# Optimization experiments

Hardware: AMD Instinct MI355X
Metric: run time of the kernel (lower is better)

Reference implementation:

```python
import jax, jax.numpy as jnp
import numpy as np


def setup_inputs() -> dict:
    key = jax.random.key(0)
    k0, k1, k2, k3, k4 = jax.random.split(key, 5)
    B, S, D, E, H = 2, 4096, 1024, 8, 512
    x = jax.random.normal(k0, (B, S, D), jnp.float32)
    w_router = jax.random.normal(k1, (D, E), jnp.float32) * (D ** -0.5)
    w1 = jax.random.normal(k2, (E, D, H), jnp.float32) * (D ** -0.5)
    w2 = jax.random.normal(k3, (E, H, D), jnp.float32) * (H ** -0.5)
    w3 = jax.random.normal(k4, (E, D, H), jnp.float32) * (D ** -0.5)
    return {"x": x, "w_router": w_router, "w1": w1, "w2": w2, "w3": w3, "top_k": 2}


def reference(x, w_router, w1, w2, w3, top_k):
    """MoE layer: linear router -> softmax -> top_k, then grouped SwiGLU experts
    combined with the routing weights. out = sum_k w_k * Expert_{idx_k}(x)."""
    B, S, D = x.shape
    E = w_router.shape[1]
    xt = x.reshape(-1, D)                              # [T, D]
    T = xt.shape[0]

    # Router
    logits = xt @ w_router                             # [T, E]
    probs = jax.nn.softmax(logits, axis=-1)
    weights, idx = jax.lax.top_k(probs, top_k)         # [T, k], [T, k]

    # Scatter top-k weights into a dense per-token gate over experts.
    gate = jnp.zeros((T, E), xt.dtype).at[jnp.arange(T)[:, None], idx].add(weights)

    h = jax.nn.silu(jnp.einsum('td,edh->teh', xt, w1)) * jnp.einsum('td,edh->teh', xt, w3)
    y = jnp.einsum('te,teh,ehd->td', gate, h, w2)      # combine
    return y.reshape(B, S, D)
```

## Files before the change

### kernel.cpp

```cpp
#include <hip/hip_runtime.h>

#define NT    8192
#define DIM   1024
#define NE    8
#define NH    512
#define NROWS (NT*2)
#define RTB   512

typedef _Float16 f16;
typedef unsigned int u32;
typedef __attribute__((ext_vector_type(8))) _Float16 f16x8;
typedef __attribute__((ext_vector_type(4))) _Float16 f16x4;
typedef __attribute__((ext_vector_type(2))) _Float16 f16x2;
typedef __attribute__((ext_vector_type(4))) float f32x4;

__device__ __forceinline__ void gl2lds16(const f16* gptr, f16* ldsptr) {
    __builtin_amdgcn_global_load_lds(
        (const __attribute__((address_space(1))) u32*)gptr,
        (__attribute__((address_space(3))) u32*)ldsptr, 16, 0, 0);
}

#define FR(sbuf, row, q) \
    (*(const f16x8*)&sbuf[(row)*32 + (((q) ^ (((row) >> 1) & 3)) << 3)])

__global__ __launch_bounds__(256) void prep_kernel(
    const float* __restrict__ x, const float* __restrict__ wr,
    const float* __restrict__ w1, const float* __restrict__ w3,
    const float* __restrict__ w2,
    f16* __restrict__ x16,
    f16* __restrict__ w1t, f16* __restrict__ w3t, f16* __restrict__ w2t,
    unsigned char* __restrict__ ge, float* __restrict__ gw,
    int* __restrict__ bhist)
{
    __shared__ float smem[NE*DIM];
    __shared__ int lhist[NE];
    int tid = threadIdx.x;
    int bi = blockIdx.x;
    if (bi < RTB) {
        if (tid < NE) lhist[tid] = 0;
        for (int i = tid; i < NE*DIM; i += 256) {
            int k = i >> 3, e = i & 7;
            smem[e*DIM + k] = wr[i];
        }
        __syncthreads();
        int tok = bi*16 + (tid >> 4);
        int kl  = tid & 15;
        float acc[NE];
        #pragma unroll
        for (int e = 0; e < NE; e++) acc[e] = 0.f;
        const float* xrow = x + (size_t)tok*DIM;
        f16* xhrow = x16 + (size_t)tok*DIM;
        #pragma unroll
        for (int i = 0; i < DIM/64; i++) {
            int kb = i*64 + kl*4;
            float4 xv = *(const float4*)(xrow + kb);
            f16x4 xh = { (f16)xv.x, (f16)xv.y, (f16)xv.z, (f16)xv.w };
            *(f16x4*)(xhrow + kb) = xh;
            #pragma unroll
            for (int e = 0; e < NE; e++) {
                float4 wv = *(const float4*)&smem[e*DIM + kb];
                acc[e] += xv.x*wv.x + xv.y*wv.y + xv.z*wv.z + xv.w*wv.w;
            }
        }
        #pragma unroll
        for (int e = 0; e < NE; e++) {
            float v = acc[e];
            v += __shfl_xor(v, 1); v += __shfl_xor(v, 2);
            v += __shfl_xor(v, 4); v += __shfl_xor(v, 8);
            acc[e] = v;
        }
        float m = acc[0];
        #pragma unroll
        for (int e = 1; e < NE; e++) m = fmaxf(m, acc[e]);
        float s = 0.f;
        #pragma unroll
        for (int e = 0; e < NE; e++) { acc[e] = __expf(acc[e] - m); s += acc[e]; }
        float inv = 1.f / s;
        int i0 = 0; float v0 = acc[0];
        #pragma unroll
        for (int e = 1; e < NE; e++) if (acc[e] > v0) { v0 = acc[e]; i0 = e; }
        int i1 = -1; float v1 = -1.f;
        #pragma unroll
        for (int e = 0; e < NE; e++) if (e != i0 && acc[e] > v1) { v1 = acc[e]; i1 = e; }
        if (kl == 0) {
            ge[2*tok+0] = (unsigned char)i0; gw[2*tok+0] = v0*inv;
            ge[2*tok+1] = (unsigned char)i1; gw[2*tok+1] = v1*inv;
        }
        #pragma unroll
        for (int ee = 0; ee < NE; ee++) {
            int c = __popcll(__ballot(kl == 0 && i0 == ee))
                  + __popcll(__ballot(kl == 0 && i1 == ee));
            if ((tid & 63) == 0 && c) atomicAdd(&lhist[ee], c);
        }
        __syncthreads();
        if (tid < NE) bhist[(size_t)bi*NE + tid] = lhist[tid];
    } else {
        int tz = bi - RTB;
        int zx = tz & 127, zy = tz >> 7;
        int tensor = zy >> 3, e = zy & 7;
        const float* src; f16* dst; int R, C;
        if (tensor == 0)      { src = w1; dst = w1t; R = DIM; C = NH; }
        else if (tensor == 1) { src = w3; dst = w3t; R = DIM; C = NH; }
        else                  { src = w2; dst = w2t; R = NH; C = DIM; }
        src += (size_t)e * DIM * NH;
        dst += (size_t)e * DIM * NH;
        int tcols = C >> 6;
        int bx = zx % tcols, by = zx / tcols;
        int r0 = by*64, c0 = bx*64;
        #pragma unroll
        for (int p = 0; p < 4; p++) {
            int r = p*16 + (tid >> 4);
            int c = (tid & 15) << 2;
            float4 v = *(const float4*)&src[(size_t)(r0 + r)*C + c0 + c];
            *(float4*)&smem[r*64 + (c ^ (((r >> 3) & 7) << 2))] = v;
        }
        __syncthreads();
        #pragma unroll
        for (int pass = 0; pass < 2; pass++) {
            int s = pass*256 + tid;
            int h = s >> 3, a = s & 7, d0 = a << 3;
            int hs = h ^ (a << 2);
            f16x8 o;
            #pragma unroll
            for (int j = 0; j < 8; j++)
                o[j] = (f16)smem[(d0 + j)*64 + hs];
            *(f16x8*)&dst[(size_t)(c0 + h)*R + r0 + d0] = o;
        }
    }
}

__global__ __launch_bounds__(256) void scatter_kernel(
    const unsigned char* __restrict__ ge, const float* __restrict__ gw,
    const int* __restrict__ bhist, int* __restrict__ offs,
    int* __restrict__ tok_ids, int* __restrict__ aid,
    float* __restrict__ row_gate)
{
    __shared__ int part_tot[32][NE], part_pre[32][NE];
    __shared__ int s_tot[NE], cur[NE];
    int tid = threadIdx.x;
    int bi = blockIdx.x;

    int e = tid & 7, c = tid >> 3;
    int lim = bi*8;
    int tot = 0, pre = 0;
    for (int b = c; b < RTB; b += 32) {
        int v = bhist[(size_t)b*NE + e];
        tot += v;
        if (b < lim) pre += v;
    }
    part_tot[c][e] = tot; part_pre[c][e] = pre;
    __syncthreads();
    if (tid < NE) {
        int t2 = 0, p2 = 0;
        #pragma unroll
        for (int c2 = 0; c2 < 32; c2++) { t2 += part_tot[c2][tid]; p2 += part_pre[c2][tid]; }
        s_tot[tid] = t2;
        part_pre[0][tid] = p2;
    }
    __syncthreads();
    int loffs[NE]; int s = 0;
    #pragma unroll
    for (int ee = 0; ee < NE; ee++) { loffs[ee] = s; s += s_tot[ee]; }
    if (bi == 0 && tid == 0) {
        #pragma unroll
        for (int ee = 0; ee < NE; ee++) offs[ee] = loffs[ee];
        offs[NE] = s;
    }
    if (tid < NE) cur[tid] = loffs[tid] + part_pre[0][tid];
    __syncthreads();

    int id = bi*256 + tid;
    int my_e = ge[id];
    float wv = gw[id];
    unsigned long long lt = (1ULL << (tid & 63)) - 1;
    int pos = 0;
    #pragma unroll
    for (int ee = 0; ee < NE; ee++) {
        unsigned long long mk = __ballot(my_e == ee);
        int cnt = __popcll(mk);
        int b = 0;
        if ((tid & 63) == 0 && cnt) b = atomicAdd(&cur[ee], cnt);
        b = __shfl(b, 0);
        if (my_e == ee) pos = b + __popcll(mk & lt);
    }
    tok_ids[pos] = id >> 1;
    aid[pos] = id;
    row_gate[pos] = wv;
}


#define BM1 128
#define BN1 64
__global__ __launch_bounds__(256,3) void gemm1_kernel(
    const f16* __restrict__ x16, const int* __restrict__ tok_ids,
    const f16* __restrict__ w1t, const f16* __restrict__ w3t,
    f16* __restrict__ gbuf, const int* __restrict__ offs)
{
    int bi = blockIdx.x;
    int e  = bi & 7;
    int r_ = bi >> 3;
    int nt = r_ & 7;
    int mt = r_ >> 3;
    int off = offs[e];
    int n_e = offs[e+1] - off;
    if (mt*BM1 >= n_e) return;

    __shared__ f16 sA [2][BM1*32];
    __shared__ f16 sB1[2][BN1*32];
    __shared__ f16 sB3[2][BN1*32];
    __shared__ int stok[BM1];

    int tid = threadIdx.x;
    if (tid < BM1) {
        int rloc = mt*BM1 + tid; rloc = rloc < n_e ? rloc : n_e - 1;
        stok[tid] = tok_ids[off + rloc];
    }
    __syncthreads();

    int lane = tid & 63, w = tid >> 6;
    int wrow = (w >> 1)*64, wcol = (w & 1)*32;
    int q = lane >> 4, lm = lane & 15;

    int lr0 = w*32 + (lane >> 2);
    int lr1 = lr0 + 16;
    int gA0 = (lane & 3) ^ ((lr0 >> 1) & 3);
    int gA1 = (lane & 3) ^ ((lr1 >> 1) & 3);
    const f16* pA0 = x16 + (size_t)stok[lr0]*DIM + gA0*8;
    const f16* pA1 = x16 + (size_t)stok[lr1]*DIM + gA1*8;
    const int lofs0 = lr0*32 + ((lane & 3) << 3);
    const int lofs1 = lr1*32 + ((lane & 3) << 3);

    int br = w*16 + (lane >> 2);
    int gB = (lane & 3) ^ ((br >> 1) & 3);
    const f16* w1p = w1t + ((size_t)e*NH + nt*BN1)*DIM;
    const f16* w3p = w3t + ((size_t)e*NH + nt*BN1)*DIM;
    const f16* pb1 = w1p + (size_t)br*DIM + gB*8;
    const f16* pb3 = w3p + (size_t)br*DIM + gB*8;
    const int bofs = br*32 + ((lane & 3) << 3);

    f32x4 acc1[4][2], acc3[4][2];
    #pragma unroll
    for (int a = 0; a < 4; a++)
        #pragma unroll
        for (int b = 0; b < 2; b++) {
            acc1[a][b] = (f32x4){0.f,0.f,0.f,0.f};
            acc3[a][b] = (f32x4){0.f,0.f,0.f,0.f};
        }

    for (int k0 = 0; k0 < DIM; k0 += 64) {
        __syncthreads();
        gl2lds16(pA0 + k0,      &sA [0][lofs0]);
        gl2lds16(pA1 + k0,      &sA [0][lofs1]);
        gl2lds16(pA0 + k0 + 32, &sA [1][lofs0]);
        gl2lds16(pA1 + k0 + 32, &sA [1][lofs1]);
        gl2lds16(pb1 + k0,      &sB1[0][bofs]);
        gl2lds16(pb1 + k0 + 32, &sB1[1][bofs]);
        gl2lds16(pb3 + k0,      &sB3[0][bofs]);
        gl2lds16(pb3 + k0 + 32, &sB3[1][bofs]);
        __syncthreads();
        #pragma unroll
        for (int ks = 0; ks < 2; ks++) {
            f16x8 aF[4], b1F[2], b3F[2];
            #pragma unroll
            for (int s = 0; s < 4; s++) aF[s] = FR(sA[ks], wrow + s*16 + lm, q);
            #pragma unroll
            for (int c = 0; c < 2; c++) {
                b1F[c] = FR(sB1[ks], wcol + c*16 + lm, q);
                b3F[c] = FR(sB3[ks], wcol + c*16 + lm, q);
            }
            #pragma unroll
            for (int sr = 0; sr < 4; sr++)
                #pragma unroll
                for (int sc = 0; sc < 2; sc++) {
                    acc1[sr][sc] = __builtin_amdgcn_mfma_f32_16x16x32_f16(aF[sr], b1F[sc], acc1[sr][sc], 0, 0, 0);
                    acc3[sr][sc] = __builtin_amdgcn_mfma_f32_16x16x32_f16(aF[sr], b3F[sc], acc3[sr][sc], 0, 0, 0);
                }
        }
    }
    #pragma unroll
    for (int sr = 0; sr < 4; sr++) {
        #pragma unroll
        for (int reg = 0; reg < 4; reg++) {
            int row = mt*BM1 + wrow + sr*16 + q*4 + reg;
            if (row < n_e) {
                #pragma unroll
                for (int sc = 0; sc < 2; sc++) {
                    int col = nt*BN1 + wcol + sc*16 + lm;
                    float h1 = acc1[sr][sc][reg];
                    float h3 = acc3[sr][sc][reg];
                    float gv = h1 / (1.f + __expf(-h1)) * h3;
                    gbuf[(size_t)(off + row)*NH + col] = (f16)gv;
                }
            }
        }
    }
}

#define BM 128
#define BN 128
__global__ __launch_bounds__(256,3) void gemm2_kernel(
    const f16* __restrict__ gbuf, const f16* __restrict__ w2t,
    const int* __restrict__ offs, const int* __restrict__ aid,
    const float* __restrict__ row_gate, f16* __restrict__ ybuf)
{
    int bi = blockIdx.x;
    int e  = bi & 7;
    int r_ = bi >> 3;
    int nt = r_ & 7;
    int mt = r_ >> 3;
    int off = offs[e];
    int n_e = offs[e+1] - off;
    if (mt*BM >= n_e) return;

    __shared__ f16 sA[2][BM*32];
    __shared__ f16 sB[2][BN*32];
    __shared__ int said[BM];
    __shared__ float sgate[BM];

    int tid = threadIdx.x;
    if (tid < BM) {
        int rloc = mt*BM + tid;
        if (rloc < n_e) { said[tid] = aid[off + rloc]; sgate[tid] = row_gate[off + rloc]; }
        else            { said[tid] = 0; sgate[tid] = 0.f; }
    }

    int lane = tid & 63, w = tid >> 6;
    int wrow = (w >> 1)*64, wcol = (w & 1)*64;
    int q = lane >> 4, lm = lane & 15;

    int lr0 = w*32 + (lane >> 2);
    int lr1 = lr0 + 16;
    int g0 = (lane & 3) ^ ((lr0 >> 1) & 3);
    int g1 = (lane & 3) ^ ((lr1 >> 1) & 3);
    int ga0 = mt*BM + lr0; ga0 = ga0 < n_e ? ga0 : n_e - 1;
    int ga1 = mt*BM + lr1; ga1 = ga1 < n_e ? ga1 : n_e - 1;
    const f16* pA0 = gbuf + (size_t)(off + ga0)*NH + g0*8;
    const f16* pA1 = gbuf + (size_t)(off + ga1)*NH + g1*8;
    const f16* w2p = w2t + ((size_t)e*DIM + nt*BN)*NH;
    const f16* pB0 = w2p + (size_t)lr0*NH + g0*8;
    const f16* pB1 = w2p + (size_t)lr1*NH + g1*8;
    const int lofs0 = lr0*32 + ((lane & 3) << 3);
    const int lofs1 = lr1*32 + ((lane & 3) << 3);

    f32x4 acc[4][4];
    #pragma unroll
    for (int a = 0; a < 4; a++)
        #pragma unroll
        for (int b = 0; b < 4; b++) acc[a][b] = (f32x4){0.f,0.f,0.f,0.f};

    __syncthreads();

    for (int k0 = 0; k0 < NH; k0 += 64) {
        gl2lds16(pA0 + k0,      &sA[0][lofs0]);
        gl2lds16(pA1 + k0,      &sA[0][lofs1]);
        gl2lds16(pA0 + k0 + 32, &sA[1][lofs0]);
        gl2lds16(pA1 + k0 + 32, &sA[1][lofs1]);
        gl2lds16(pB0 + k0,      &sB[0][lofs0]);
        gl2lds16(pB1 + k0,      &sB[0][lofs1]);
        gl2lds16(pB0 + k0 + 32, &sB[1][lofs0]);
        gl2lds16(pB1 + k0 + 32, &sB[1][lofs1]);
        __syncthreads();
        #pragma unroll
        for (int ks = 0; ks < 2; ks++) {
            f16x8 aF[4], bF[4];
            #pragma unroll
            for (int s = 0; s < 4; s++) {
                aF[s] = FR(sA[ks], wrow + s*16 + lm, q);
                bF[s] = FR(sB[ks], wcol + s*16 + lm, q);
            }
            #pragma unroll
            for (int sr = 0; sr < 4; sr++)
                #pragma unroll
                for (int sc = 0; sc < 4; sc++)
                    acc[sr][sc] = __builtin_amdgcn_mfma_f32_16x16x32_f16(aF[sr], bF[sc], acc[sr][sc], 0, 0, 0);
        }
        __syncthreads();
    }
    #pragma unroll
    for (int sr = 0; sr < 4; sr++) {
        #pragma unroll
        for (int reg = 0; reg < 4; reg++) {
            int lrow = wrow + sr*16 + q*4 + reg;
            if (mt*BM + lrow < n_e) {
                int id = said[lrow];
                float wgt = sgate[lrow];
                #pragma unroll
                for (int sc = 0; sc < 4; sc++) {
                    int col = nt*BN + wcol + sc*16 + lm;
                    ybuf[(size_t)id*DIM + col] = (f16)(wgt * acc[sr][sc][reg]);
                }
            }
        }
    }
}

__global__ __launch_bounds__(256) void combine_kernel(
    const f16* __restrict__ ybuf, float* __restrict__ out)
{
    int gid = blockIdx.x*256 + threadIdx.x;
    int t = gid >> 7;
    int c = (gid & 127) << 3;
    f16x8 y0 = *(const f16x8*)(ybuf + ((size_t)2*t)*DIM + c);
    f16x8 y1 = *(const f16x8*)(ybuf + ((size_t)2*t+1)*DIM + c);
    float* op = out + (size_t)t*DIM + c;
    float4 o0 = { (float)y0[0] + (float)y1[0], (float)y0[1] + (float)y1[1],
                  (float)y0[2] + (float)y1[2], (float)y0[3] + (float)y1[3] };
    float4 o1 = { (float)y0[4] + (float)y1[4], (float)y0[5] + (float)y1[5],
                  (float)y0[6] + (float)y1[6], (float)y0[7] + (float)y1[7] };
    *(float4*)op = o0;
    *(float4*)(op + 4) = o1;
}

extern "C" void kernel_launch(void* const* d_in, const int* in_sizes, int n_in,
                              void* d_out, int out_size, void* d_ws, size_t ws_size,
                              hipStream_t stream)
{
    const float* x  = (const float*)d_in[0];
    const float* wr = (const float*)d_in[1];
    const float* w1 = (const float*)d_in[2];
    const float* w2 = (const float*)d_in[3];
    const float* w3 = (const float*)d_in[4];
    float* out = (float*)d_out;

    char* ws = (char*)d_ws;
    f16* ybuf    = (f16*)ws;        ws += (size_t)NROWS*DIM*sizeof(f16);
    f16* w1t     = (f16*)ws;        ws += (size_t)NE*NH*DIM*sizeof(f16);
    f16* w3t     = (f16*)ws;        ws += (size_t)NE*NH*DIM*sizeof(f16);
    f16* w2t     = (f16*)ws;        ws += (size_t)NE*DIM*NH*sizeof(f16);
    f16* gbuf    = (f16*)ws;        ws += (size_t)NROWS*NH*sizeof(f16);
    int* tok_ids = (int*)ws;        ws += (size_t)NROWS*4;
    int* aid     = (int*)ws;        ws += (size_t)NROWS*4;
    float* row_gate = (float*)ws;   ws += (size_t)NROWS*4;
    int* offs    = (int*)ws;        ws += 64;
    unsigned char* ge = (unsigned char*)ws; ws += (size_t)NROWS;
    float* gw    = (float*)ws;      ws += (size_t)NROWS*4;
    int* bhist   = (int*)ws;        ws += (size_t)RTB*NE*4;
    if (ws_size < (size_t)(ws - (char*)d_ws)) return;

    f16* x16 = ybuf;

    prep_kernel<<<RTB + 3072, 256, 0, stream>>>(x, wr, w1, w3, w2,
                                                x16, w1t, w3t, w2t,
                                                ge, gw, bhist);
    scatter_kernel<<<NROWS/256, 256, 0, stream>>>(ge, gw, bhist, offs,
                                                  tok_ids, aid, row_gate);
    gemm1_kernel<<<4096, 256, 0, stream>>>(x16, tok_ids, w1t, w3t, gbuf, offs);
    gemm2_kernel<<<8192, 256, 0, stream>>>(gbuf, w2t, offs, aid, row_gate, ybuf);
    combine_kernel<<<(NT*(DIM/8))/256, 256, 0, stream>>>(ybuf, out);
}
```

Before: 221.0 us.

## Fuse top-2 combine into gemm2 epilogue via per-token atomic tickets

Removes the separate combine kernel. Each gemm2 tile writes its gated fp16 result to ybuf, then takes a ticket on a per-token, per-64-column counter. The second of the two expert contributions to arrive reads its partner's row and writes the fp32 sum to the output. This saves one kernel launch and a full pass over ybuf. In exchange it adds atomics, thread fences and scattered partner reads, and correctness depends on the fences ordering the ybuf writes correctly.

```diff
diff --git a/kernel.cpp b/kernel.cpp
--- a/kernel.cpp
+++ b/kernel.cpp
@@ -30,13 +30,14 @@
     f16* __restrict__ x16,
     f16* __restrict__ w1t, f16* __restrict__ w3t, f16* __restrict__ w2t,
     unsigned char* __restrict__ ge, float* __restrict__ gw,
-    int* __restrict__ bhist)
+    int* __restrict__ bhist, u32* __restrict__ tick)
 {
     __shared__ float smem[NE*DIM];
     __shared__ int lhist[NE];
     int tid = threadIdx.x;
     int bi = blockIdx.x;
     if (bi < RTB) {
+        tick[bi*256 + tid] = 0;
         if (tid < NE) lhist[tid] = 0;
         for (int i = tid; i < NE*DIM; i += 256) {
             int k = i >> 3, e = i & 7;
@@ -301,7 +302,8 @@
 __global__ __launch_bounds__(256,3) void gemm2_kernel(
     const f16* __restrict__ gbuf, const f16* __restrict__ w2t,
     const int* __restrict__ offs, const int* __restrict__ aid,
-    const float* __restrict__ row_gate, f16* __restrict__ ybuf)
+    const float* __restrict__ row_gate, f16* __restrict__ ybuf,
+    u32* __restrict__ tick, float* __restrict__ out)
 {
     int bi = blockIdx.x;
     int e  = bi & 7;
@@ -376,6 +378,7 @@
         }
         __syncthreads();
     }
+
     #pragma unroll
     for (int sr = 0; sr < 4; sr++) {
         #pragma unroll
@@ -387,28 +390,52 @@
                 #pragma unroll
                 for (int sc = 0; sc < 4; sc++) {
                     int col = nt*BN + wcol + sc*16 + lm;
-                    ybuf[(size_t)id*DIM + col] = (f16)(wgt * acc[sr][sc][reg]);
+                    f16 v16 = (f16)(wgt * acc[sr][sc][reg]);
+                    ybuf[(size_t)id*DIM + col] = v16;
+                    acc[sr][sc][reg] = (float)v16;
                 }
             }
         }
     }
-}
-
-__global__ __launch_bounds__(256) void combine_kernel(
-    const f16* __restrict__ ybuf, float* __restrict__ out)
-{
-    int gid = blockIdx.x*256 + threadIdx.x;
-    int t = gid >> 7;
-    int c = (gid & 127) << 3;
-    f16x8 y0 = *(const f16x8*)(ybuf + ((size_t)2*t)*DIM + c);
-    f16x8 y1 = *(const f16x8*)(ybuf + ((size_t)2*t+1)*DIM + c);
-    float* op = out + (size_t)t*DIM + c;
-    float4 o0 = { (float)y0[0] + (float)y1[0], (float)y0[1] + (float)y1[1],
-                  (float)y0[2] + (float)y1[2], (float)y0[3] + (float)y1[3] };
-    float4 o1 = { (float)y0[4] + (float)y1[4], (float)y0[5] + (float)y1[5],
-                  (float)y0[6] + (float)y1[6], (float)y0[7] + (float)y1[7] };
-    *(float4*)op = o0;
-    *(float4*)(op + 4) = o1;
+    __threadfence();
+
+    int colh = nt*2 + (wcol >> 6);
+    unsigned need = 0;
+    #pragma unroll
+    for (int sr = 0; sr < 4; sr++) {
+        #pragma unroll
+        for (int reg = 0; reg < 4; reg++) {
+            int lrow = wrow + sr*16 + q*4 + reg;
+            if (mt*BM + lrow < n_e) {
+                int t = said[lrow] >> 1;
+                u32 old = 0;
+                if (lm == 0) old = atomicAdd(&tick[t*16 + colh], 1u);
+                old = __shfl(old, q << 4);
+                if (old == 1) need |= 1u << (sr*4 + reg);
+            }
+        }
+    }
+
+    if (need) {
+        __threadfence();
+        #pragma unroll
+        for (int sr = 0; sr < 4; sr++) {
+            #pragma unroll
+            for (int reg = 0; reg < 4; reg++) {
+                if (need & (1u << (sr*4 + reg))) {
+                    int lrow = wrow + sr*16 + q*4 + reg;
+                    int id = said[lrow];
+                    int t = id >> 1, pid = id ^ 1;
+                    #pragma unroll
+                    for (int sc = 0; sc < 4; sc++) {
+                        int col = nt*BN + wcol + sc*16 + lm;
+                        float p = (float)ybuf[(size_t)pid*DIM + col];
+                        out[(size_t)t*DIM + col] = p + acc[sr][sc][reg];
+                    }
+                }
+            }
+        }
+    }
 }
 
 extern "C" void kernel_launch(void* const* d_in, const int* in_sizes, int n_in,
@@ -435,16 +462,17 @@
     unsigned char* ge = (unsigned char*)ws; ws += (size_t)NROWS;
     float* gw    = (float*)ws;      ws += (size_t)NROWS*4;
     int* bhist   = (int*)ws;        ws += (size_t)RTB*NE*4;
+    u32* tick    = (u32*)ws;        ws += (size_t)NT*16*4;
     if (ws_size < (size_t)(ws - (char*)d_ws)) return;
 
     f16* x16 = ybuf;
 
     prep_kernel<<<RTB + 3072, 256, 0, stream>>>(x, wr, w1, w3, w2,
                                                 x16, w1t, w3t, w2t,
-                                                ge, gw, bhist);
+                                                ge, gw, bhist, tick);
     scatter_kernel<<<NROWS/256, 256, 0, stream>>>(ge, gw, bhist, offs,
                                                   tok_ids, aid, row_gate);
     gemm1_kernel<<<4096, 256, 0, stream>>>(x16, tok_ids, w1t, w3t, gbuf, offs);
-    gemm2_kernel<<<8192, 256, 0, stream>>>(gbuf, w2t, offs, aid, row_gate, ybuf);
-    combine_kernel<<<(NT*(DIM/8))/256, 256, 0, stream>>>(ybuf, out);
-}
+    gemm2_kernel<<<8192, 256, 0, stream>>>(gbuf, w2t, offs, aid, row_gate,
+                                           ybuf, tick, out);
+}
```

New measurement: 531.8 us. 2.41x slower.

## Fuse token scatter into gemm1 by locating routed rows from block histograms

Applied to the files above, without the earlier changes.

Drops the separate scatter kernel. Each gemm1 block now rebuilds the expert offsets from the per-block histogram and finds its own routed tokens by prefix search over the histogram and the expert-id bytes. Blocks with nt==0 also write tok_ids, aid and row_gate for gemm2. This saves one launch and its serialization point, but every gemm1 block now does redundant histogram reads and a serial search before starting its GEMM work. Row order within an expert changes from the old atomic order to token-id order.

```diff
diff --git a/kernel.cpp b/kernel.cpp
--- a/kernel.cpp
+++ b/kernel.cpp
@@ -129,91 +129,108 @@
     }
 }
 
-__global__ __launch_bounds__(256) void scatter_kernel(
-    const unsigned char* __restrict__ ge, const float* __restrict__ gw,
-    const int* __restrict__ bhist, int* __restrict__ offs,
-    int* __restrict__ tok_ids, int* __restrict__ aid,
-    float* __restrict__ row_gate)
-{
-    __shared__ int part_tot[32][NE], part_pre[32][NE];
-    __shared__ int s_tot[NE], cur[NE];
-    int tid = threadIdx.x;
-    int bi = blockIdx.x;
-
-    int e = tid & 7, c = tid >> 3;
-    int lim = bi*8;
-    int tot = 0, pre = 0;
-    for (int b = c; b < RTB; b += 32) {
-        int v = bhist[(size_t)b*NE + e];
-        tot += v;
-        if (b < lim) pre += v;
-    }
-    part_tot[c][e] = tot; part_pre[c][e] = pre;
-    __syncthreads();
-    if (tid < NE) {
-        int t2 = 0, p2 = 0;
-        #pragma unroll
-        for (int c2 = 0; c2 < 32; c2++) { t2 += part_tot[c2][tid]; p2 += part_pre[c2][tid]; }
-        s_tot[tid] = t2;
-        part_pre[0][tid] = p2;
-    }
-    __syncthreads();
-    int loffs[NE]; int s = 0;
-    #pragma unroll
-    for (int ee = 0; ee < NE; ee++) { loffs[ee] = s; s += s_tot[ee]; }
-    if (bi == 0 && tid == 0) {
-        #pragma unroll
-        for (int ee = 0; ee < NE; ee++) offs[ee] = loffs[ee];
-        offs[NE] = s;
-    }
-    if (tid < NE) cur[tid] = loffs[tid] + part_pre[0][tid];
-    __syncthreads();
-
-    int id = bi*256 + tid;
-    int my_e = ge[id];
-    float wv = gw[id];
-    unsigned long long lt = (1ULL << (tid & 63)) - 1;
-    int pos = 0;
-    #pragma unroll
-    for (int ee = 0; ee < NE; ee++) {
-        unsigned long long mk = __ballot(my_e == ee);
-        int cnt = __popcll(mk);
-        int b = 0;
-        if ((tid & 63) == 0 && cnt) b = atomicAdd(&cur[ee], cnt);
-        b = __shfl(b, 0);
-        if (my_e == ee) pos = b + __popcll(mk & lt);
-    }
-    tok_ids[pos] = id >> 1;
-    aid[pos] = id;
-    row_gate[pos] = wv;
-}
-
 
 #define BM1 128
 #define BN1 64
 __global__ __launch_bounds__(256,3) void gemm1_kernel(
-    const f16* __restrict__ x16, const int* __restrict__ tok_ids,
+    const f16* __restrict__ x16, const unsigned char* __restrict__ ge,
+    const float* __restrict__ gw, const int* __restrict__ bhist,
     const f16* __restrict__ w1t, const f16* __restrict__ w3t,
-    f16* __restrict__ gbuf, const int* __restrict__ offs)
+    f16* __restrict__ gbuf, int* __restrict__ offs,
+    int* __restrict__ tok_ids, int* __restrict__ aid,
+    float* __restrict__ row_gate)
 {
     int bi = blockIdx.x;
     int e  = bi & 7;
     int r_ = bi >> 3;
     int nt = r_ & 7;
     int mt = r_ >> 3;
-    int off = offs[e];
-    int n_e = offs[e+1] - off;
-    if (mt*BM1 >= n_e) return;
-
+    int tid = threadIdx.x;
+
+    __shared__ int ptot[32][NE];
+    __shared__ int stot[NE];
+    __shared__ int csum[33];
     __shared__ f16 sA [2][BM1*32];
     __shared__ f16 sB1[2][BN1*32];
     __shared__ f16 sB3[2][BN1*32];
     __shared__ int stok[BM1];
 
-    int tid = threadIdx.x;
+    {
+        int e_ = tid & 7, cc = tid >> 3;
+        int t = 0;
+        for (int b = cc; b < RTB; b += 32) t += bhist[b*NE + e_];
+        ptot[cc][e_] = t;
+    }
+    __syncthreads();
+    if (tid < NE) {
+        int s = 0;
+        #pragma unroll
+        for (int c2 = 0; c2 < 32; c2++) s += ptot[c2][tid];
+        stot[tid] = s;
+    }
+    __syncthreads();
+    int loffs[NE]; int tot = 0;
+    #pragma unroll
+    for (int ee = 0; ee < NE; ee++) { loffs[ee] = tot; tot += stot[ee]; }
+    if (bi == 0 && tid == 0) {
+        #pragma unroll
+        for (int ee = 0; ee < NE; ee++) offs[ee] = loffs[ee];
+        offs[NE] = tot;
+    }
+    int off = loffs[e];
+    int n_e = stot[e];
+    if (mt*BM1 >= n_e) return;
+
+    if (tid < 32) {
+        int s = 0;
+        #pragma unroll
+        for (int j = 0; j < 16; j++) s += bhist[(tid*16 + j)*NE + e];
+        csum[tid] = s;
+    }
+    __syncthreads();
+    if (tid == 0) {
+        int s = 0;
+        #pragma unroll
+        for (int c2 = 0; c2 < 32; c2++) { int v = csum[c2]; csum[c2] = s; s += v; }
+        csum[32] = s;
+    }
+    __syncthreads();
+
     if (tid < BM1) {
-        int rloc = mt*BM1 + tid; rloc = rloc < n_e ? rloc : n_e - 1;
-        stok[tid] = tok_ids[off + rloc];
+        int r = mt*BM1 + tid;
+        int un = (r < n_e);
+        if (!un) r = n_e - 1;
+        int lo = 0;
+        #pragma unroll
+        for (int c2 = 1; c2 < 32; c2++) if (csum[c2] <= r) lo = c2;
+        int hv[16];
+        #pragma unroll
+        for (int j = 0; j < 16; j++) hv[j] = bhist[(lo*16 + j)*NE + e];
+        int rem = r - csum[lo];
+        int b = lo*16, done = 0;
+        #pragma unroll
+        for (int j = 0; j < 16; j++) {
+            if (!done) { if (rem >= hv[j]) { rem -= hv[j]; b++; } else done = 1; }
+        }
+        const uint4* gp = (const uint4*)(ge + b*32);
+        uint4 g0 = gp[0], g1 = gp[1];
+        u32 gwd[8] = { g0.x, g0.y, g0.z, g0.w, g1.x, g1.y, g1.z, g1.w };
+        int k = rem, found = b*32;
+        int searching = 1;
+        #pragma unroll
+        for (int j = 0; j < 32; j++) {
+            int eb = (gwd[j >> 2] >> ((j & 3)*8)) & 0xff;
+            if (searching && eb == e) {
+                if (k == 0) { found = b*32 + j; searching = 0; }
+                else k--;
+            }
+        }
+        stok[tid] = found >> 1;
+        if (un && nt == 0) {
+            tok_ids[off + r] = found >> 1;
+            aid[off + r] = found;
+            row_gate[off + r] = gw[found];
+        }
     }
     __syncthreads();
 
@@ -242,9 +259,9 @@
     #pragma unroll
     for (int a = 0; a < 4; a++)
         #pragma unroll
-        for (int b = 0; b < 2; b++) {
-            acc1[a][b] = (f32x4){0.f,0.f,0.f,0.f};
-            acc3[a][b] = (f32x4){0.f,0.f,0.f,0.f};
+        for (int b2 = 0; b2 < 2; b2++) {
+            acc1[a][b2] = (f32x4){0.f,0.f,0.f,0.f};
+            acc3[a][b2] = (f32x4){0.f,0.f,0.f,0.f};
         }
 
     for (int k0 = 0; k0 < DIM; k0 += 64) {
@@ -442,9 +459,8 @@
     prep_kernel<<<RTB + 3072, 256, 0, stream>>>(x, wr, w1, w3, w2,
                                                 x16, w1t, w3t, w2t,
                                                 ge, gw, bhist);
-    scatter_kernel<<<NROWS/256, 256, 0, stream>>>(ge, gw, bhist, offs,
-                                                  tok_ids, aid, row_gate);
-    gemm1_kernel<<<4096, 256, 0, stream>>>(x16, tok_ids, w1t, w3t, gbuf, offs);
+    gemm1_kernel<<<4096, 256, 0, stream>>>(x16, ge, gw, bhist, w1t, w3t,
+                                           gbuf, offs, tok_ids, aid, row_gate);
     gemm2_kernel<<<8192, 256, 0, stream>>>(gbuf, w2t, offs, aid, row_gate, ybuf);
     combine_kernel<<<(NT*(DIM/8))/256, 256, 0, stream>>>(ybuf, out);
 }
```

Result: no change. 223.8 us (+1.3%).
